# Kernel tuning notes

Hardware: AMD Instinct MI355X
Metric: run time of the kernel (lower is better)

The kernel has to match this reference:

```python
import jax, jax.numpy as jnp
import numpy as np

LOG_2PI = np.float32(np.log(2.0 * np.pi))
NEG_BIG = np.float32(-9e15)


def setup_inputs() -> dict:
    key = jax.random.key(0)
    ks = jax.random.split(key, 8)
    N, F_in, F_out, H = 8192, 512, 128, 16
    x = jax.random.normal(ks[0], (N, F_in), dtype=jnp.float32)
    adj = jax.random.randint(ks[1], (N, N), 0, 2, dtype=jnp.int32)
    # xavier_uniform-ish init for W (gain 1.414)
    lim = np.float32(1.414 * np.sqrt(6.0 / (F_in + F_out)))
    W = jax.random.uniform(ks[2], (F_in, F_out), jnp.float32, -lim, lim)
    # VariationalAttentionNet params: lin1(2*F_out -> H), lin21/lin22(H -> 1)
    w1 = jax.random.normal(ks[3], (H, 2 * F_out), dtype=jnp.float32) * 0.05
    b1 = jnp.zeros((H,), jnp.float32)
    w21 = jax.random.normal(ks[4], (1, H), dtype=jnp.float32) * 0.05
    b21 = jnp.zeros((1,), jnp.float32)
    w22 = jax.random.normal(ks[5], (1, H), dtype=jnp.float32) * 0.05
    b22 = jnp.zeros((1,), jnp.float32)
    return {"x": x, "adj": adj, "W": W, "w1": w1, "b1": b1,
            "w21": w21, "b21": b21, "w22": w22, "b22": b22}


def reference(x, adj, W, w1, b1, w21, b21, w22, b22):
    # h = x @ W  [N, F_out]
    h = x @ W
    # VariationalAttentionNet(h, h), eval mode: z = mu
    u = jax.nn.relu(jnp.concatenate([h, h], axis=1) @ w1.T + b1)  # [N, H]
    mu = u @ w21.T + b21   # [N, 1]
    lv = u @ w22.T + b22   # [N, 1]
    sigma = jax.nn.softplus(lv)
    z = mu
    # qmp = -(log p(z) - log q(z)); with z = mu, log q(mu) = -log(sigma) - 0.5*log(2pi)
    log_p = jnp.sum(-0.5 * z * z - 0.5 * LOG_2PI)
    log_q = jnp.sum(-jnp.log(sigma) - 0.5 * LOG_2PI)
    qmp = log_q - log_p
    # per-node score z broadcast across row, masked by adjacency, row softmax
    scores = jnp.where(adj > 0, z, NEG_BIG)          # [N, N]
    attention = jax.nn.softmax(scores, axis=1)       # [N, N] (dropout off in eval)
    h_prime = attention @ h                          # [N, F_out]
    return jax.nn.elu(h_prime), qmp
```

## Files before the change

kernel.cpp:

```cpp
#include <hip/hip_runtime.h>

typedef unsigned int u32;
typedef unsigned short u16;

#define NN 8192
#define FIN 512
#define FOUT 128
#define NH 16
#define BK 64
#define BKA 256

typedef float f32x16 __attribute__((ext_vector_type(16)));
typedef __bf16 bf16x8 __attribute__((ext_vector_type(8)));

union PackAB { u32 u[4]; bf16x8 v; };

__device__ __forceinline__ u32 rne_hi(u32 u) {
  return u + (0x7FFFu + ((u >> 16) & 1u));
}
__device__ __forceinline__ u16 f32_to_bf16(float f) {
  return (u16)(rne_hi(__float_as_uint(f)) >> 16);
}

__global__ __launch_bounds__(256) void prep_kernel(
    const float* __restrict__ W, const float* __restrict__ w1,
    u16* __restrict__ WT, float* __restrict__ w1s) {
  int b = blockIdx.x, t = threadIdx.x;
  if (b < 256) {
    int o = b * 256 + t;
    int n = o >> 9, k = o & 511;
    WT[o] = f32_to_bf16(W[k * FOUT + n]);
  } else {
    for (int e = t; e < NH * FOUT; e += 256) {
      int k = e >> 7, f = e & 127;
      w1s[e] = w1[k * 256 + f] + w1[k * 256 + 128 + f];
    }
  }
}

__global__ __launch_bounds__(256, 6) void h_kernel(
    const float* __restrict__ x, const u16* __restrict__ WT,
    float* __restrict__ Hp, int KL) {
  __shared__ u16 aS[32 * BK];
  __shared__ u16 bS[128 * BK];
  int t = threadIdx.x;
  int w = t >> 6, l = t & 63;
  int m = l & 31, kh = l >> 5;
  int tile = blockIdx.x & 255, chunk = blockIdx.x >> 8;
  int i0 = tile * 32, k0 = chunk * KL;

  int arow = t >> 4, acol = (t & 15) * 4;
  int ac = (t & 15) >> 1, ah = t & 1;
  int aoff0 = arow * BK + ((ac ^ (arow & 7)) << 3) + ah * 4;
  int aoff1 = (arow + 16) * BK + ((ac ^ ((arow + 16) & 7)) << 3) + ah * 4;
  const float* ap0 = x + (size_t)(i0 + arow) * FIN + k0 + acol;
  const float* ap1 = ap0 + (size_t)16 * FIN;
  int hr = t >> 3, hc = t & 7;
  const u16* bp0 = WT + (size_t)hr * FIN + k0 + hc * 8;
  int boff[4];
#pragma unroll
  for (int p = 0; p < 4; ++p) {
    int r = hr + 32 * p;
    boff[p] = r * BK + ((hc ^ (r & 7)) << 3);
  }
  int aro = m * BK, am7 = m & 7;
  int nB = w * 32 + m;
  int bro = nB * BK, bm7 = nB & 7;

  f32x16 acc;
#pragma unroll
  for (int r = 0; r < 16; ++r) acc[r] = 0.0f;

  for (int o = 0; o < KL; o += BK) {
    float4 a0 = *(const float4*)ap0;
    float4 a1 = *(const float4*)ap1;
    uint4 h0 = *(const uint4*)bp0;
    uint4 h1 = *(const uint4*)(bp0 + 32 * (size_t)FIN);
    uint4 h2 = *(const uint4*)(bp0 + 64 * (size_t)FIN);
    uint4 h3 = *(const uint4*)(bp0 + 96 * (size_t)FIN);
    ap0 += BK; ap1 += BK; bp0 += BK;
    uint2 w0, w1v;
    w0.x = (rne_hi(__float_as_uint(a0.y)) & 0xFFFF0000u) | (rne_hi(__float_as_uint(a0.x)) >> 16);
    w0.y = (rne_hi(__float_as_uint(a0.w)) & 0xFFFF0000u) | (rne_hi(__float_as_uint(a0.z)) >> 16);
    w1v.x = (rne_hi(__float_as_uint(a1.y)) & 0xFFFF0000u) | (rne_hi(__float_as_uint(a1.x)) >> 16);
    w1v.y = (rne_hi(__float_as_uint(a1.w)) & 0xFFFF0000u) | (rne_hi(__float_as_uint(a1.z)) >> 16);
    *(uint2*)&aS[aoff0] = w0;
    *(uint2*)&aS[aoff1] = w1v;
    *(uint4*)&bS[boff[0]] = h0;
    *(uint4*)&bS[boff[1]] = h1;
    *(uint4*)&bS[boff[2]] = h2;
    *(uint4*)&bS[boff[3]] = h3;
    __syncthreads();
#pragma unroll
    for (int s = 0; s < BK; s += 16) {
      int cA = (s >> 3) + kh;
      PackAB pa, pb;
      pa.v = *(const bf16x8*)&aS[aro + ((cA ^ am7) << 3)];
      pb.v = *(const bf16x8*)&bS[bro + ((cA ^ bm7) << 3)];
      acc = __builtin_amdgcn_mfma_f32_32x32x16_bf16(pa.v, pb.v, acc, 0, 0, 0);
    }
    __syncthreads();
  }
  float* hp = Hp + (size_t)chunk * NN * FOUT;
  int col = w * 32 + m;
#pragma unroll
  for (int r = 0; r < 16; ++r) {
    int row = (r & 3) + 8 * (r >> 2) + 4 * kh;
    hp[(size_t)(i0 + row) * FOUT + col] = acc[r];
  }
}

__global__ __launch_bounds__(256) void reduceH_kernel(
    const float* __restrict__ Hp, int KSH,
    const float* __restrict__ b1, const float* __restrict__ w21,
    const float* __restrict__ b21, const float* __restrict__ w22,
    const float* __restrict__ b22, const float* __restrict__ w1s,
    u16* __restrict__ HTf, float* __restrict__ qpart) {
  __shared__ float hs[32][FOUT + 4];
  __shared__ float w1l[NH][FOUT + 4];
  __shared__ float us[32][NH + 1];
  int t = threadIdx.x;
  int i0 = blockIdx.x * 32;
  float v[16];
  const float* base = Hp + (size_t)i0 * FOUT + t * 16;
#pragma unroll
  for (int e = 0; e < 16; e += 4) {
    float4 x4 = *(const float4*)(base + e);
    v[e] = x4.x; v[e + 1] = x4.y; v[e + 2] = x4.z; v[e + 3] = x4.w;
  }
  for (int c = 1; c < KSH; ++c) {
    const float* p = base + (size_t)c * NN * FOUT;
#pragma unroll
    for (int e = 0; e < 16; e += 4) {
      float4 x4 = *(const float4*)(p + e);
      v[e] += x4.x; v[e + 1] += x4.y; v[e + 2] += x4.z; v[e + 3] += x4.w;
    }
  }
  {
    int row = t >> 3, c0 = (t & 7) * 16;
#pragma unroll
    for (int e = 0; e < 16; ++e) hs[row][c0 + e] = v[e];
  }
  for (int e = t; e < NH * FOUT; e += 256) w1l[e >> 7][e & 127] = w1s[e];
  __syncthreads();
  {
    int n = t & 127, g2 = t >> 7;
#pragma unroll
    for (int gg = 0; gg < 2; ++gg) {
      int g = g2 + 2 * gg;
      int k16 = (i0 >> 4) + (g >> 1), kh = g & 1;
      u32 p[4];
#pragma unroll
      for (int j = 0; j < 4; ++j) {
        u16 lo = f32_to_bf16(hs[g * 8 + 2 * j][n]);
        u16 hi = f32_to_bf16(hs[g * 8 + 2 * j + 1][n]);
        p[j] = (u32)lo | ((u32)hi << 16);
      }
      uint4 st; st.x = p[0]; st.y = p[1]; st.z = p[2]; st.w = p[3];
      size_t off = ((size_t)(k16 * 4 + (n >> 5)) * 64 + kh * 32 + (n & 31)) * 8;
      *(uint4*)(HTf + off) = st;
    }
  }
  {
    int i = t >> 3, p = t & 7;
    float s0 = b1[p], s1 = b1[p + 8];
#pragma unroll 4
    for (int f = 0; f < FOUT; ++f) {
      float hv = hs[i][f];
      s0 = fmaf(hv, w1l[p][f], s0);
      s1 = fmaf(hv, w1l[p + 8][f], s1);
    }
    us[i][p] = fmaxf(s0, 0.0f);
    us[i][p + 8] = fmaxf(s1, 0.0f);
  }
  __syncthreads();
  if (t < 32) {
    float mu = b21[0], lv = b22[0];
#pragma unroll
    for (int k = 0; k < NH; ++k) {
      mu = fmaf(us[t][k], w21[k], mu);
      lv = fmaf(us[t][k], w22[k], lv);
    }
    float sp = fmaxf(lv, 0.0f) + log1pf(expf(-fabsf(lv)));
    float q = 0.5f * mu * mu - logf(sp);
#pragma unroll
    for (int off = 16; off; off >>= 1) q += __shfl_down(q, off);
    if (t == 0) qpart[blockIdx.x] = q;
  }
}

__global__ __launch_bounds__(256, 4) void attn_kernel(
    const int* __restrict__ adj, const u16* __restrict__ HTf,
    float* __restrict__ Sp, u32* __restrict__ degw, int KL) {
  __shared__ u16 aS[32 * BKA];
  int t = threadIdx.x;
  int w = t >> 6, l = t & 63;
  int m = l & 31, kh = l >> 5;
  int tile = blockIdx.x & 255, chunk = blockIdx.x >> 8;
  int i0 = tile * 32, k0 = chunk * KL;

  int ar = t >> 3, lc = t & 7;
  const int* apb = adj + (size_t)(i0 + ar) * NN + k0 + lc * 4;
  int woff[8];
#pragma unroll
  for (int q = 0; q < 8; ++q) {
    int c = q * 4 + (lc >> 1);
    woff[q] = ar * 256 + (((c ^ ar) & 31) << 3) + (lc & 1) * 4;
  }
  const u16* bp = HTf + ((size_t)(k0 >> 4) * 4 * 64 + (size_t)(w * 64 + l)) * 8;

  f32x16 acc;
#pragma unroll
  for (int r = 0; r < 16; ++r) acc[r] = 0.0f;
  u32 degacc = 0;

  int nslab = KL / BKA;
  int4 aC[8], aN[8];
#pragma unroll
  for (int q = 0; q < 8; ++q) aC[q] = *(const int4*)(apb + q * 32);
  apb += BKA;

  for (int o = 0; o < nslab; ++o) {
    if (o) __syncthreads();
#pragma unroll
    for (int q = 0; q < 8; ++q) {
      u32 p0 = ((u32)aC[q].y << 16) | (u32)aC[q].x;
      u32 p1 = ((u32)aC[q].w << 16) | (u32)aC[q].z;
      degacc += p0 + p1;
      uint2 wv; wv.x = p0 * 0x3F80u; wv.y = p1 * 0x3F80u;
      *(uint2*)&aS[woff[q]] = wv;
    }
    __syncthreads();
    if (o + 1 < nslab) {
#pragma unroll
      for (int q = 0; q < 8; ++q) aN[q] = *(const int4*)(apb + q * 32);
      apb += BKA;
    }
    {
      bf16x8 bF[4];
#pragma unroll
      for (int j = 0; j < 4; ++j) bF[j] = *(const bf16x8*)(bp + j * 2048);
#pragma unroll
      for (int k16 = 0; k16 < 16; k16 += 4) {
        bf16x8 bN[4];
        if (k16 + 4 < 16) {
#pragma unroll
          for (int j = 0; j < 4; ++j)
            bN[j] = *(const bf16x8*)(bp + (k16 + 4 + j) * 2048);
        }
#pragma unroll
        for (int j = 0; j < 4; ++j) {
          int cc = (k16 + j) * 2 + kh;
          PackAB pa;
          pa.v = *(const bf16x8*)&aS[m * 256 + (((cc ^ m) & 31) << 3)];
          acc = __builtin_amdgcn_mfma_f32_32x32x16_bf16(pa.v, bF[j], acc, 0, 0, 0);
        }
#pragma unroll
        for (int j = 0; j < 4; ++j) bF[j] = bN[j];
      }
    }
    bp += (size_t)16 * 2048;
#pragma unroll
    for (int q = 0; q < 8; ++q) aC[q] = aN[q];
  }
  u32 d = (degacc & 0xFFFFu) + (degacc >> 16);
  d += __shfl_down(d, 4);
  d += __shfl_down(d, 2);
  d += __shfl_down(d, 1);
  if (lc == 0) degw[chunk * NN + i0 + ar] = d;
  float* sp = Sp + (size_t)chunk * NN * FOUT;
  int col = w * 32 + m;
#pragma unroll
  for (int r = 0; r < 16; ++r) {
    int row = (r & 3) + 8 * (r >> 2) + 4 * kh;
    sp[(size_t)(i0 + row) * FOUT + col] = acc[r];
  }
}

__global__ __launch_bounds__(256) void reduceSq_kernel(
    const float* __restrict__ Sp, const u32* __restrict__ degw,
    const float* __restrict__ qpart, float* __restrict__ out, int KSA) {
  int t = threadIdx.x;
  if (blockIdx.x == 1024) {
    __shared__ float sred[4];
    float v = qpart[t];
#pragma unroll
    for (int off = 32; off; off >>= 1) v += __shfl_down(v, off);
    if ((t & 63) == 0) sred[t >> 6] = v;
    __syncthreads();
    if (t == 0) out[(size_t)NN * FOUT] = sred[0] + sred[1] + sred[2] + sred[3];
    return;
  }
  int idx = (blockIdx.x * 256 + t) * 4;
  int i = idx >> 7;
  u32 deg = 0;
  for (int c = 0; c < KSA; ++c) deg += degw[c * NN + i];
  float4 s = {0.0f, 0.0f, 0.0f, 0.0f};
  for (int c = 0; c < KSA; ++c) {
    float4 v4 = *(const float4*)(Sp + (size_t)c * NN * FOUT + idx);
    s.x += v4.x; s.y += v4.y; s.z += v4.z; s.w += v4.w;
  }
  float rd = deg ? 1.0f / (float)deg : 0.0f;
  float4 o;
  o.x = s.x * rd; o.y = s.y * rd; o.z = s.z * rd; o.w = s.w * rd;
  o.x = o.x > 0.0f ? o.x : expm1f(o.x);
  o.y = o.y > 0.0f ? o.y : expm1f(o.y);
  o.z = o.z > 0.0f ? o.z : expm1f(o.z);
  o.w = o.w > 0.0f ? o.w : expm1f(o.w);
  *(float4*)(out + idx) = o;
}

extern "C" void kernel_launch(void* const* d_in, const int* in_sizes, int n_in,
                              void* d_out, int out_size, void* d_ws, size_t ws_size,
                              hipStream_t stream) {
  (void)in_sizes; (void)n_in; (void)out_size;
  const float* x   = (const float*)d_in[0];
  const int*   adj = (const int*)d_in[1];
  const float* W   = (const float*)d_in[2];
  const float* w1  = (const float*)d_in[3];
  const float* b1  = (const float*)d_in[4];
  const float* w21 = (const float*)d_in[5];
  const float* b21 = (const float*)d_in[6];
  const float* w22 = (const float*)d_in[7];
  const float* b22 = (const float*)d_in[8];
  float* out = (float*)d_out;

  const size_t TILE4 = (size_t)NN * FOUT * 4;
  int KSA = 4, KSH = 4;
  for (;;) {
    size_t need = (size_t)(KSA + KSH) * TILE4
                + (size_t)NN * FOUT * 2
                + (size_t)FOUT * FIN * 2
                + (size_t)KSA * NN * 4
                + NH * FOUT * 4 + 2048;
    if (need <= ws_size || (KSA == 1 && KSH == 1)) break;
    if (KSH > 1) KSH >>= 1; else KSA >>= 1;
  }

  char* ws = (char*)d_ws;
  float* Sp   = (float*)ws;                          ws += (size_t)KSA * TILE4;
  float* Hp   = (float*)ws;                          ws += (size_t)KSH * TILE4;
  u16*   HTf  = (u16*)ws;                            ws += (size_t)NN * FOUT * 2;
  u16*   WT   = (u16*)ws;                            ws += (size_t)FOUT * FIN * 2;
  u32*   degw = (u32*)ws;                            ws += (size_t)KSA * NN * 4;
  float* w1s  = (float*)ws;                          ws += NH * FOUT * 4;
  float* qpart= (float*)ws;

  prep_kernel<<<257, 256, 0, stream>>>(W, w1, WT, w1s);
  h_kernel<<<256 * KSH, 256, 0, stream>>>(x, WT, Hp, FIN / KSH);
  reduceH_kernel<<<256, 256, 0, stream>>>(Hp, KSH, b1, w21, b21, w22, b22, w1s, HTf, qpart);
  attn_kernel<<<256 * KSA, 256, 0, stream>>>(adj, HTf, Sp, degw, NN / KSA);
  reduceSq_kernel<<<1025, 256, 0, stream>>>(Sp, degw, qpart, out, KSA);
}
```

Measured before the change: 418.0 us.

## Double-buffer adjacency LDS tile and switch to k-major LDS layout

The attention GEMM kernel now keeps two LDS buffers for the bf16-converted adjacency slab. Each iteration runs its MFMAs on one buffer while converting and storing the next slab into the other, cutting the per-slab barrier count from two to one. The LDS layout changes from row-major with an XOR swizzle to a k-major arrangement, so MFMA operand reads become contiguous per lane. In exchange LDS use doubles, which may affect the 4-blocks-per-CU occupancy target, and the new write pattern may cause bank conflicts.

```diff
diff --git a/kernel.cpp b/kernel.cpp
--- a/kernel.cpp
+++ b/kernel.cpp
@@ -192,7 +192,7 @@
 __global__ __launch_bounds__(256, 4) void attn_kernel(
     const int* __restrict__ adj, const u16* __restrict__ HTf,
     float* __restrict__ Sp, u32* __restrict__ degw, int KL) {
-  __shared__ u16 aS[32 * BKA];
+  __shared__ u16 aS[2][8192];
   int t = threadIdx.x;
   int w = t >> 6, l = t & 63;
   int m = l & 31, kh = l >> 5;
@@ -203,11 +203,10 @@
   const int* apb = adj + (size_t)(i0 + ar) * NN + k0 + lc * 4;
   int woff[8];
 #pragma unroll
-  for (int q = 0; q < 8; ++q) {
-    int c = q * 4 + (lc >> 1);
-    woff[q] = ar * 256 + (((c ^ ar) & 31) << 3) + (lc & 1) * 4;
-  }
-  const u16* bp = HTf + ((size_t)(k0 >> 4) * 4 * 64 + (size_t)(w * 64 + l)) * 8;
+  for (int q = 0; q < 8; ++q)
+    woff[q] = (q * 4 + (lc >> 1)) * 256 + ar * 8 + (lc & 1) * 4;
+  const u16* bp = HTf + ((size_t)(k0 >> 4) * 256 + (size_t)(w * 64 + l)) * 8;
+  int rdo = l * 8;
 
   f32x16 acc;
 #pragma unroll
@@ -215,53 +214,64 @@
   u32 degacc = 0;
 
   int nslab = KL / BKA;
-  int4 aC[8], aN[8];
+  int4 aC[8];
 #pragma unroll
   for (int q = 0; q < 8; ++q) aC[q] = *(const int4*)(apb + q * 32);
   apb += BKA;
+#pragma unroll
+  for (int q = 0; q < 8; ++q) {
+    u32 p0 = ((u32)aC[q].y << 16) | (u32)aC[q].x;
+    u32 p1 = ((u32)aC[q].w << 16) | (u32)aC[q].z;
+    degacc += p0 + p1;
+    uint2 wv; wv.x = p0 * 0x3F80u; wv.y = p1 * 0x3F80u;
+    *(uint2*)&aS[0][woff[q]] = wv;
+  }
+  if (nslab > 1) {
+#pragma unroll
+    for (int q = 0; q < 8; ++q) aC[q] = *(const int4*)(apb + q * 32);
+    apb += BKA;
+  }
+  __syncthreads();
 
   for (int o = 0; o < nslab; ++o) {
-    if (o) __syncthreads();
-#pragma unroll
-    for (int q = 0; q < 8; ++q) {
-      u32 p0 = ((u32)aC[q].y << 16) | (u32)aC[q].x;
-      u32 p1 = ((u32)aC[q].w << 16) | (u32)aC[q].z;
-      degacc += p0 + p1;
-      uint2 wv; wv.x = p0 * 0x3F80u; wv.y = p1 * 0x3F80u;
-      *(uint2*)&aS[woff[q]] = wv;
-    }
-    __syncthreads();
+    int bsel = o & 1;
+    bf16x8 bF[4];
+#pragma unroll
+    for (int j = 0; j < 4; ++j) bF[j] = *(const bf16x8*)(bp + j * 2048);
+#pragma unroll
+    for (int k16 = 0; k16 < 16; k16 += 4) {
+      bf16x8 bN[4];
+      if (k16 + 4 < 16) {
+#pragma unroll
+        for (int j = 0; j < 4; ++j)
+          bN[j] = *(const bf16x8*)(bp + (k16 + 4 + j) * 2048);
+      }
+#pragma unroll
+      for (int j = 0; j < 4; ++j) {
+        PackAB pa;
+        pa.v = *(const bf16x8*)&aS[bsel][(k16 + j) * 512 + rdo];
+        acc = __builtin_amdgcn_mfma_f32_32x32x16_bf16(pa.v, bF[j], acc, 0, 0, 0);
+      }
+#pragma unroll
+      for (int j = 0; j < 4; ++j) bF[j] = bN[j];
+    }
+    bp += (size_t)16 * 2048;
     if (o + 1 < nslab) {
 #pragma unroll
-      for (int q = 0; q < 8; ++q) aN[q] = *(const int4*)(apb + q * 32);
-      apb += BKA;
-    }
-    {
-      bf16x8 bF[4];
-#pragma unroll
-      for (int j = 0; j < 4; ++j) bF[j] = *(const bf16x8*)(bp + j * 2048);
-#pragma unroll
-      for (int k16 = 0; k16 < 16; k16 += 4) {
-        bf16x8 bN[4];
-        if (k16 + 4 < 16) {
-#pragma unroll
-          for (int j = 0; j < 4; ++j)
-            bN[j] = *(const bf16x8*)(bp + (k16 + 4 + j) * 2048);
-        }
-#pragma unroll
-        for (int j = 0; j < 4; ++j) {
-          int cc = (k16 + j) * 2 + kh;
-          PackAB pa;
-          pa.v = *(const bf16x8*)&aS[m * 256 + (((cc ^ m) & 31) << 3)];
-          acc = __builtin_amdgcn_mfma_f32_32x32x16_bf16(pa.v, bF[j], acc, 0, 0, 0);
-        }
-#pragma unroll
-        for (int j = 0; j < 4; ++j) bF[j] = bN[j];
-      }
-    }
-    bp += (size_t)16 * 2048;
-#pragma unroll
-    for (int q = 0; q < 8; ++q) aC[q] = aN[q];
+      for (int q = 0; q < 8; ++q) {
+        u32 p0 = ((u32)aC[q].y << 16) | (u32)aC[q].x;
+        u32 p1 = ((u32)aC[q].w << 16) | (u32)aC[q].z;
+        degacc += p0 + p1;
+        uint2 wv; wv.x = p0 * 0x3F80u; wv.y = p1 * 0x3F80u;
+        *(uint2*)&aS[bsel ^ 1][woff[q]] = wv;
+      }
+      if (o + 2 < nslab) {
+#pragma unroll
+        for (int q = 0; q < 8; ++q) aC[q] = *(const int4*)(apb + q * 32);
+        apb += BKA;
+      }
+      __syncthreads();
+    }
   }
   u32 d = (degacc & 0xFFFFu) + (degacc >> 16);
   d += __shfl_down(d, 4);
```

Result: no change. 422.7 us (+1.1%).
